# Performance work log

Measured on AMD Instinct MI355X. Metric: run time of the kernel, lower is better.

## Reference

```python
import jax, jax.numpy as jnp
import numpy as np

MIN_NORM = 1e-15
PROJ_EPS = 4e-3  # fp32 eps used by hgcn PoincareBall


def _artanh(x):
    x = jnp.clip(x, -1.0 + 1e-7, 1.0 - 1e-7)
    return 0.5 * jnp.log((1.0 + x) / (1.0 - x))


def _norm(x):
    return jnp.maximum(jnp.linalg.norm(x, axis=-1, keepdims=True), MIN_NORM)


def proj(x, c):
    norm = _norm(x)
    maxnorm = (1.0 - PROJ_EPS) / jnp.sqrt(c)
    return jnp.where(norm > maxnorm, x / norm * maxnorm, x)


def expmap0(u, c):
    sqrt_c = jnp.sqrt(c)
    u_norm = _norm(u)
    return jnp.tanh(sqrt_c * u_norm) * u / (sqrt_c * u_norm)


def logmap0(p, c):
    sqrt_c = jnp.sqrt(c)
    p_norm = _norm(p)
    return _artanh(sqrt_c * p_norm) * p / (sqrt_c * p_norm)


def mobius_add(x, y, c):
    x2 = jnp.sum(x * x, axis=-1, keepdims=True)
    y2 = jnp.sum(y * y, axis=-1, keepdims=True)
    xy = jnp.sum(x * y, axis=-1, keepdims=True)
    num = (1.0 + 2.0 * c * xy + c * y2) * x + (1.0 - c * x2) * y
    denom = 1.0 + 2.0 * c * xy + c * c * x2 * y2
    return num / jnp.maximum(denom, MIN_NORM)


def mobius_matvec(m, x, c):
    sqrt_c = jnp.sqrt(c)
    x_norm = _norm(x)
    mx = x @ m.T  # [N, out]
    mx_norm = _norm(mx)
    res_c = jnp.tanh(mx_norm / x_norm * _artanh(sqrt_c * x_norm)) * mx / (mx_norm * sqrt_c)
    cond = jnp.all(mx == 0.0, axis=-1, keepdims=True)
    return jnp.where(cond, jnp.zeros_like(res_c), res_c)


def setup_inputs() -> dict:
    key = jax.random.key(0)
    k1, k2, k3 = jax.random.split(key, 3)
    N, D = 8192, 256
    c = 1.0
    x = 0.05 * jax.random.normal(k1, (N, D), dtype=jnp.float32)
    x = proj(x, c)  # valid points on the Poincare ball
    # sparse-ish row-normalized adjacency, materialized densely
    a = (jax.random.uniform(k2, (N, N)) < 0.004).astype(jnp.float32)
    a = a + jnp.eye(N, dtype=jnp.float32)
    adj = a / jnp.sum(a, axis=-1, keepdims=True)
    gain = np.sqrt(2.0)
    bound = gain * np.sqrt(6.0 / (D + D))  # xavier_uniform with gain sqrt(2)
    weight = jax.random.uniform(k3, (D, D), minval=-bound, maxval=bound, dtype=jnp.float32)
    bias = jnp.zeros((D,), dtype=jnp.float32)
    return {"x": x, "adj": adj, "weight": weight, "bias": bias}


def reference(x, adj, weight, bias):
    c_in = jnp.float32(1.0)
    c_out = jnp.float32(1.0)
    # HypLinear (dropout=0, eval mode)
    mv = mobius_matvec(weight, x, c_in)
    res = proj(mv, c_in)
    hyp_bias = proj(expmap0(bias[None, :], c_in), c_in)  # proj_tan0 is identity
    h = proj(mobius_add(res, hyp_bias, c_in), c_in)
    # HypAgg (use_att=False): tangent-space neighborhood aggregation
    x_tangent = logmap0(h, c_in)
    support_t = adj @ x_tangent
    h = proj(expmap0(support_t, c_in), c_in)
    # HypAct
    xt = jax.nn.relu(logmap0(h, c_in))
    h = proj(expmap0(xt, c_out), c_out)
    return (h, adj)
```

## Files before the change

kernel.cpp:

```cpp
#include <hip/hip_runtime.h>
#include <hip/hip_bf16.h>

#define N_NODES 8192
#define D_DIM   256

typedef __attribute__((ext_vector_type(8))) short short8v;
typedef __attribute__((ext_vector_type(4))) float f32x4;

__device__ __forceinline__ float artanh_clip(float x) {
    x = fminf(x, 1.0f - 1e-7f);
    return 0.5f * logf((1.0f + x) / (1.0f - x));
}

__device__ __forceinline__ ushort4 cvt4_bf16(float4 v) {
    ushort4 b;
    b.x = __bfloat16_as_ushort(__float2bfloat16(v.x));
    b.y = __bfloat16_as_ushort(__float2bfloat16(v.y));
    b.z = __bfloat16_as_ushort(__float2bfloat16(v.z));
    b.w = __bfloat16_as_ushort(__float2bfloat16(v.w));
    return b;
}

__global__ void k0_bias(const float* __restrict__ bias, float* __restrict__ hbg) {
    __shared__ float sp[4];
    __shared__ float s_g;
    int t = threadIdx.x;
    float u = bias[t];
    float v = u * u;
    #pragma unroll
    for (int o = 1; o < 64; o <<= 1) v += __shfl_xor(v, o);
    if ((t & 63) == 0) sp[t >> 6] = v;
    __syncthreads();
    if (t == 0) {
        float s  = sp[0] + sp[1] + sp[2] + sp[3];
        float un = fmaxf(sqrtf(s), 1e-15f);
        float t1 = tanhf(un);
        s_g = (t1 > 0.996f) ? (0.996f / un) : (t1 / un);
    }
    __syncthreads();
    float hb = s_g * u;
    hbg[t] = hb;
    float v2 = hb * hb;
    #pragma unroll
    for (int o = 1; o < 64; o <<= 1) v2 += __shfl_xor(v2, o);
    if ((t & 63) == 0) sp[t >> 6] = v2;
    __syncthreads();
    if (t == 0) hbg[256] = sp[0] + sp[1] + sp[2] + sp[3];
}

__global__ __launch_bounds__(256) void k1_hyplinear(
    const float* __restrict__ x, const float* __restrict__ W,
    const float* __restrict__ hbg, __hip_bfloat16* __restrict__ xtT)
{
    __shared__ __align__(16) float sw[256][36];
    __shared__ __align__(16) float smx[16][260];
    __shared__ float s_xn[16], s_P[16], s_Q[16];
    __shared__ float s_hb[256];
    __shared__ float s_b2;

    const int t  = threadIdx.x;
    const int r0 = blockIdx.x * 16;

    s_hb[t] = hbg[t];
    if (t == 0) s_b2 = hbg[256];

    {
        int r = t >> 4, j = t & 15;
        const float* xp = x + (r0 + r) * 256 + j * 16;
        float s2 = 0.f;
        #pragma unroll
        for (int i = 0; i < 4; i++) {
            float4 v = *(const float4*)(xp + 4 * i);
            s2 += v.x * v.x + v.y * v.y + v.z * v.z + v.w * v.w;
        }
        s2 += __shfl_xor(s2, 1); s2 += __shfl_xor(s2, 2);
        s2 += __shfl_xor(s2, 4); s2 += __shfl_xor(s2, 8);
        if (j == 0) s_xn[r] = s2;
    }

    float acc[16];
    #pragma unroll
    for (int r = 0; r < 16; r++) acc[r] = 0.f;

    for (int kc = 0; kc < 8; kc++) {
        __syncthreads();
        {
            int c4 = (t & 7) * 4;
            #pragma unroll
            for (int i = 0; i < 8; i++) {
                int d = i * 32 + (t >> 3);
                *(float4*)(&sw[d][c4]) = *(const float4*)(W + d * 256 + kc * 32 + c4);
            }
        }
        __syncthreads();
        #pragma unroll
        for (int kk = 0; kk < 8; kk++) {
            float4 w4 = *(const float4*)(&sw[t][kk * 4]);
            #pragma unroll
            for (int r = 0; r < 16; r++) {
                const float4 xv = *(const float4*)(x + (r0 + r) * 256 + kc * 32 + kk * 4);
                acc[r] = fmaf(xv.x, w4.x, acc[r]);
                acc[r] = fmaf(xv.y, w4.y, acc[r]);
                acc[r] = fmaf(xv.z, w4.z, acc[r]);
                acc[r] = fmaf(xv.w, w4.w, acc[r]);
            }
        }
    }
    __syncthreads();
    #pragma unroll
    for (int r = 0; r < 16; r++) smx[r][t] = acc[r];
    __syncthreads();

    {
        int r = t >> 4, j = t & 15;
        float s2 = 0.f, dt = 0.f;
        #pragma unroll
        for (int i = 0; i < 16; i++) {
            float v = smx[r][j + 16 * i];
            s2 += v * v;
            dt += v * s_hb[j + 16 * i];
        }
        s2 += __shfl_xor(s2, 1); s2 += __shfl_xor(s2, 2);
        s2 += __shfl_xor(s2, 4); s2 += __shfl_xor(s2, 8);
        dt += __shfl_xor(dt, 1); dt += __shfl_xor(dt, 2);
        dt += __shfl_xor(dt, 4); dt += __shfl_xor(dt, 8);
        if (j == 0) {
            float b2  = s_b2;
            float xn  = fmaxf(sqrtf(s_xn[r]), 1e-15f);
            float mx2 = s2;
            float mxn = fmaxf(sqrtf(mx2), 1e-15f);
            float at = artanh_clip(xn);
            float tt = tanhf(mxn / xn * at);
            float fr = tt / mxn;
            if (tt > 0.996f) fr = 0.996f / mxn;
            float mvn = fminf(tt, 0.996f);
            float x2  = mvn * mvn;
            float xy  = fr * dt;
            float cA  = 1.0f + 2.0f * xy + b2;
            float cB  = 1.0f - x2;
            float den = fmaxf(1.0f + 2.0f * xy + x2 * b2, 1e-15f);
            float P0 = cA * fr / den;
            float Q0 = cB / den;
            float hn = sqrtf(fmaxf(P0 * P0 * mx2 + 2.0f * P0 * Q0 * dt + Q0 * Q0 * b2, 0.0f));
            hn = fmaxf(hn, 1e-15f);
            float pf  = (hn > 0.996f) ? (0.996f / hn) : 1.0f;
            float hnp = fminf(hn, 0.996f);
            float lam = artanh_clip(hnp) / hnp;
            s_P[r] = lam * pf * P0;
            s_Q[r] = lam * pf * Q0;
        }
    }
    __syncthreads();

    {
        float hb = s_hb[t];
        unsigned int pk[8];
        #pragma unroll
        for (int r = 0; r < 16; r += 2) {
            float a0 = s_P[r]     * acc[r]     + s_Q[r]     * hb;
            float a1 = s_P[r + 1] * acc[r + 1] + s_Q[r + 1] * hb;
            unsigned int lo = (unsigned int)__bfloat16_as_ushort(__float2bfloat16(a0));
            unsigned int hi = (unsigned int)__bfloat16_as_ushort(__float2bfloat16(a1));
            pk[r >> 1] = lo | (hi << 16);
        }
        uint4* dst = (uint4*)(xtT + t * 8192 + r0);
        dst[0] = make_uint4(pk[0], pk[1], pk[2], pk[3]);
        dst[1] = make_uint4(pk[4], pk[5], pk[6], pk[7]);
    }
}

__global__ __launch_bounds__(512) void k2_agg(
    const float* __restrict__ adj,
    const __hip_bfloat16* __restrict__ xtT,
    float* __restrict__ out_h,
    float* __restrict__ out_adj)
{
    __shared__ __align__(16) __hip_bfloat16 As[2][32][72];

    const int t     = threadIdx.x;
    const int lane  = t & 63;
    const int wave  = t >> 6;
    const int wr    = wave >> 2;
    const int wc    = wave & 3;
    const int bx    = blockIdx.x;
    const int m0    = (bx >> 2) * 32;
    const int kbase = (bx & 3) * 2048;

    const int srow = t >> 4;
    const int scol = (t & 15) * 4;
    const float* astage = adj     + (m0 + srow) * 8192 + kbase + scol;
    float*       ostage = out_adj + (m0 + srow) * 8192 + kbase + scol;

    const int arow = lane & 15;
    const int g8   = 8 * (lane >> 4);
    const int acol = wr * 32 + g8;
    const __hip_bfloat16* bptr = xtT + (wc * 64 + arow) * 8192 + kbase + wr * 32 + g8;

    f32x4 acc[8];
    #pragma unroll
    for (int i = 0; i < 8; i++) acc[i] = (f32x4){0.f, 0.f, 0.f, 0.f};

    {
        float4 v = *(const float4*)(astage);
        *(float4*)(ostage) = v;
        *(ushort4*)(&As[0][srow][scol]) = cvt4_bf16(v);
    }
    __syncthreads();

    for (int kt = 0; kt < 32; kt++) {
        const int cur = kt & 1;
        const bool hn = (kt + 1 < 32);
        float4 v;
        if (hn) v = *(const float4*)(astage + (kt + 1) * 64);

        const __hip_bfloat16* bb = bptr + kt * 64;
        short8v b0 = *(const short8v*)(bb);
        short8v b1 = *(const short8v*)(bb + 16 * 8192);
        short8v b2 = *(const short8v*)(bb + 32 * 8192);
        short8v b3 = *(const short8v*)(bb + 48 * 8192);
        short8v a0 = *(const short8v*)(&As[cur][arow][acol]);
        short8v a1 = *(const short8v*)(&As[cur][16 + arow][acol]);

        acc[0] = __builtin_amdgcn_mfma_f32_16x16x32_bf16(a0, b0, acc[0], 0, 0, 0);
        acc[1] = __builtin_amdgcn_mfma_f32_16x16x32_bf16(a0, b1, acc[1], 0, 0, 0);
        acc[2] = __builtin_amdgcn_mfma_f32_16x16x32_bf16(a0, b2, acc[2], 0, 0, 0);
        acc[3] = __builtin_amdgcn_mfma_f32_16x16x32_bf16(a0, b3, acc[3], 0, 0, 0);
        acc[4] = __builtin_amdgcn_mfma_f32_16x16x32_bf16(a1, b0, acc[4], 0, 0, 0);
        acc[5] = __builtin_amdgcn_mfma_f32_16x16x32_bf16(a1, b1, acc[5], 0, 0, 0);
        acc[6] = __builtin_amdgcn_mfma_f32_16x16x32_bf16(a1, b2, acc[6], 0, 0, 0);
        acc[7] = __builtin_amdgcn_mfma_f32_16x16x32_bf16(a1, b3, acc[7], 0, 0, 0);

        if (hn) {
            *(float4*)(ostage + (kt + 1) * 64) = v;
            *(ushort4*)(&As[cur ^ 1][srow][scol]) = cvt4_bf16(v);
        }
        __syncthreads();
    }

    const int crow0 = 4 * (lane >> 4);
    const int ccol  = lane & 15;
    #pragma unroll
    for (int mf = 0; mf < 2; mf++)
        #pragma unroll
        for (int nf = 0; nf < 4; nf++)
            #pragma unroll
            for (int q = 0; q < 4; q++)
                atomicAdd(out_h + (m0 + mf * 16 + crow0 + q) * 256 + wc * 64 + nf * 16 + ccol,
                          acc[mf * 4 + nf][q]);
}

__global__ __launch_bounds__(256) void k3_epilogue(float* __restrict__ h) {
    const int t = threadIdx.x;
    const int r = blockIdx.x * 16 + (t >> 4);
    const int j = t & 15;
    float* p = h + r * 256 + j * 16;

    float4 v[4];
    float s2 = 0.f, sp = 0.f;
    #pragma unroll
    for (int i = 0; i < 4; i++) {
        v[i] = *(const float4*)(p + 4 * i);
        s2 += v[i].x * v[i].x + v[i].y * v[i].y + v[i].z * v[i].z + v[i].w * v[i].w;
        float px = fmaxf(v[i].x, 0.f), py = fmaxf(v[i].y, 0.f);
        float pz = fmaxf(v[i].z, 0.f), pw = fmaxf(v[i].w, 0.f);
        sp += px * px + py * py + pz * pz + pw * pw;
    }
    s2 += __shfl_xor(s2, 1); s2 += __shfl_xor(s2, 2); s2 += __shfl_xor(s2, 4); s2 += __shfl_xor(s2, 8);
    sp += __shfl_xor(sp, 1); sp += __shfl_xor(sp, 2); sp += __shfl_xor(sp, 4); sp += __shfl_xor(sp, 8);

    float ns = fmaxf(sqrtf(s2), 1e-15f);
    float t1 = tanhf(ns);
    float alpha = (t1 > 0.996f) ? (0.996f / ns) : (t1 / ns);
    float nh = fminf(t1, 0.996f);
    float beta = artanh_clip(nh) / nh;
    float ba = beta * alpha;
    float nxt = fmaxf(ba * sqrtf(sp), 1e-15f);
    float t2 = tanhf(nxt);
    float delta = (t2 > 0.996f) ? (0.996f / nxt) : (t2 / nxt);
    float F = delta * ba;

    #pragma unroll
    for (int i = 0; i < 4; i++) {
        float4 o;
        o.x = F * fmaxf(v[i].x, 0.f);
        o.y = F * fmaxf(v[i].y, 0.f);
        o.z = F * fmaxf(v[i].z, 0.f);
        o.w = F * fmaxf(v[i].w, 0.f);
        *(float4*)(p + 4 * i) = o;
    }
}

extern "C" void kernel_launch(void* const* d_in, const int* in_sizes, int n_in,
                              void* d_out, int out_size, void* d_ws, size_t ws_size,
                              hipStream_t stream)
{
    const float* x    = (const float*)d_in[0];
    const float* adj  = (const float*)d_in[1];
    const float* W    = (const float*)d_in[2];
    const float* bias = (const float*)d_in[3];

    float* out_h   = (float*)d_out;
    float* out_adj = out_h + (size_t)N_NODES * D_DIM;

    __hip_bfloat16* xtT = (__hip_bfloat16*)d_ws;
    float* hbg = (float*)((char*)d_ws + (size_t)D_DIM * N_NODES * 2);

    k0_bias<<<1, 256, 0, stream>>>(bias, hbg);
    k1_hyplinear<<<512, 256, 0, stream>>>(x, W, hbg, xtT);
    hipMemsetAsync(out_h, 0, (size_t)N_NODES * D_DIM * sizeof(float), stream);
    k2_agg<<<1024, 512, 0, stream>>>(adj, xtT, out_h, out_adj);
    k3_epilogue<<<512, 256, 0, stream>>>(out_h);
}
```

Measured before the change: 304.8 us.

## Replace split-K atomic aggregation with column-tiled full-K GEMM and stage x in LDS

The aggregation kernel no longer splits K across four blocks with atomicAdd. Each block now covers a 32-row by 64-column output tile over the full K range and writes its result directly, so the memset is removed. The copy of adj to the output now uses nontemporal stores. In the linear kernel, x is staged once in shared memory instead of being re-read from global memory inside the FMA loop. The trade-off is that the four column blocks of each row tile each re-read the adj tile and each rewrite the same out_adj region, which multiplies the main memory traffic.

```diff
diff --git a/kernel.cpp b/kernel.cpp
--- a/kernel.cpp
+++ b/kernel.cpp
@@ -21,6 +21,11 @@
     return b;
 }
 
+__device__ __forceinline__ void nt_store4(float4 v, float* p) {
+    f32x4 w = {v.x, v.y, v.z, v.w};
+    __builtin_nontemporal_store(w, (f32x4*)p);
+}
+
 __global__ void k0_bias(const float* __restrict__ bias, float* __restrict__ hbg) {
     __shared__ float sp[4];
     __shared__ float s_g;
@@ -52,27 +57,32 @@
     const float* __restrict__ x, const float* __restrict__ W,
     const float* __restrict__ hbg, __hip_bfloat16* __restrict__ xtT)
 {
+    __shared__ __align__(16) float sx[16][264];
     __shared__ __align__(16) float sw[256][36];
-    __shared__ __align__(16) float smx[16][260];
     __shared__ float s_xn[16], s_P[16], s_Q[16];
     __shared__ float s_hb[256];
     __shared__ float s_b2;
 
     const int t  = threadIdx.x;
     const int r0 = blockIdx.x * 16;
-
+    const int row = t >> 4;
+    const int j16 = (t & 15) * 4;
+
+    {
+        #pragma unroll
+        for (int i = 0; i < 4; i++)
+            *(float4*)(&sx[row][j16 + 64 * i]) =
+                *(const float4*)(x + (r0 + row) * 256 + j16 + 64 * i);
+    }
     s_hb[t] = hbg[t];
     if (t == 0) s_b2 = hbg[256];
+    __syncthreads();
 
     {
         int r = t >> 4, j = t & 15;
-        const float* xp = x + (r0 + r) * 256 + j * 16;
         float s2 = 0.f;
         #pragma unroll
-        for (int i = 0; i < 4; i++) {
-            float4 v = *(const float4*)(xp + 4 * i);
-            s2 += v.x * v.x + v.y * v.y + v.z * v.z + v.w * v.w;
-        }
+        for (int i = 0; i < 16; i++) { float v = sx[r][j + 16 * i]; s2 += v * v; }
         s2 += __shfl_xor(s2, 1); s2 += __shfl_xor(s2, 2);
         s2 += __shfl_xor(s2, 4); s2 += __shfl_xor(s2, 8);
         if (j == 0) s_xn[r] = s2;
@@ -98,17 +108,17 @@
             float4 w4 = *(const float4*)(&sw[t][kk * 4]);
             #pragma unroll
             for (int r = 0; r < 16; r++) {
-                const float4 xv = *(const float4*)(x + (r0 + r) * 256 + kc * 32 + kk * 4);
-                acc[r] = fmaf(xv.x, w4.x, acc[r]);
-                acc[r] = fmaf(xv.y, w4.y, acc[r]);
-                acc[r] = fmaf(xv.z, w4.z, acc[r]);
-                acc[r] = fmaf(xv.w, w4.w, acc[r]);
+                float4 x4 = *(const float4*)(&sx[r][kc * 32 + kk * 4]);
+                acc[r] = fmaf(x4.x, w4.x, acc[r]);
+                acc[r] = fmaf(x4.y, w4.y, acc[r]);
+                acc[r] = fmaf(x4.z, w4.z, acc[r]);
+                acc[r] = fmaf(x4.w, w4.w, acc[r]);
             }
         }
     }
     __syncthreads();
     #pragma unroll
-    for (int r = 0; r < 16; r++) smx[r][t] = acc[r];
+    for (int r = 0; r < 16; r++) sx[r][t] = acc[r];
     __syncthreads();
 
     {
@@ -116,7 +126,7 @@
         float s2 = 0.f, dt = 0.f;
         #pragma unroll
         for (int i = 0; i < 16; i++) {
-            float v = smx[r][j + 16 * i];
+            float v = sx[r][j + 16 * i];
             s2 += v * v;
             dt += v * s_hb[j + 16 * i];
         }
@@ -177,61 +187,51 @@
 {
     __shared__ __align__(16) __hip_bfloat16 As[2][32][72];
 
-    const int t     = threadIdx.x;
-    const int lane  = t & 63;
-    const int wave  = t >> 6;
-    const int wr    = wave >> 2;
-    const int wc    = wave & 3;
-    const int bx    = blockIdx.x;
-    const int m0    = (bx >> 2) * 32;
-    const int kbase = (bx & 3) * 2048;
+    const int t    = threadIdx.x;
+    const int lane = t & 63;
+    const int wave = t >> 6;
+    const int wrh  = wave >> 2;
+    const int wc   = wave & 3;
+    const int bx   = blockIdx.x;
+    const int m    = (bx >> 5) * 8 + (bx & 7);
+    const int c    = (bx >> 3) & 3;
+    const int m0   = m * 32;
+    const int n0   = c * 64;
 
     const int srow = t >> 4;
     const int scol = (t & 15) * 4;
-    const float* astage = adj     + (m0 + srow) * 8192 + kbase + scol;
-    float*       ostage = out_adj + (m0 + srow) * 8192 + kbase + scol;
+    const float* astage = adj     + (m0 + srow) * 8192 + scol;
+    float*       ostage = out_adj + (m0 + srow) * 8192 + scol;
 
     const int arow = lane & 15;
     const int g8   = 8 * (lane >> 4);
-    const int acol = wr * 32 + g8;
-    const __hip_bfloat16* bptr = xtT + (wc * 64 + arow) * 8192 + kbase + wr * 32 + g8;
-
-    f32x4 acc[8];
-    #pragma unroll
-    for (int i = 0; i < 8; i++) acc[i] = (f32x4){0.f, 0.f, 0.f, 0.f};
+    const __hip_bfloat16* bptr = xtT + (n0 + wc * 16 + arow) * 8192 + g8;
+
+    f32x4 acc = (f32x4){0.f, 0.f, 0.f, 0.f};
 
     {
         float4 v = *(const float4*)(astage);
-        *(float4*)(ostage) = v;
+        nt_store4(v, ostage);
         *(ushort4*)(&As[0][srow][scol]) = cvt4_bf16(v);
     }
     __syncthreads();
 
-    for (int kt = 0; kt < 32; kt++) {
+    for (int kt = 0; kt < 128; kt++) {
         const int cur = kt & 1;
-        const bool hn = (kt + 1 < 32);
+        const bool hn = (kt + 1 < 128);
         float4 v;
         if (hn) v = *(const float4*)(astage + (kt + 1) * 64);
 
-        const __hip_bfloat16* bb = bptr + kt * 64;
-        short8v b0 = *(const short8v*)(bb);
-        short8v b1 = *(const short8v*)(bb + 16 * 8192);
-        short8v b2 = *(const short8v*)(bb + 32 * 8192);
-        short8v b3 = *(const short8v*)(bb + 48 * 8192);
-        short8v a0 = *(const short8v*)(&As[cur][arow][acol]);
-        short8v a1 = *(const short8v*)(&As[cur][16 + arow][acol]);
-
-        acc[0] = __builtin_amdgcn_mfma_f32_16x16x32_bf16(a0, b0, acc[0], 0, 0, 0);
-        acc[1] = __builtin_amdgcn_mfma_f32_16x16x32_bf16(a0, b1, acc[1], 0, 0, 0);
-        acc[2] = __builtin_amdgcn_mfma_f32_16x16x32_bf16(a0, b2, acc[2], 0, 0, 0);
-        acc[3] = __builtin_amdgcn_mfma_f32_16x16x32_bf16(a0, b3, acc[3], 0, 0, 0);
-        acc[4] = __builtin_amdgcn_mfma_f32_16x16x32_bf16(a1, b0, acc[4], 0, 0, 0);
-        acc[5] = __builtin_amdgcn_mfma_f32_16x16x32_bf16(a1, b1, acc[5], 0, 0, 0);
-        acc[6] = __builtin_amdgcn_mfma_f32_16x16x32_bf16(a1, b2, acc[6], 0, 0, 0);
-        acc[7] = __builtin_amdgcn_mfma_f32_16x16x32_bf16(a1, b3, acc[7], 0, 0, 0);
+        short8v b0 = *(const short8v*)(bptr + kt * 64);
+        short8v b1 = *(const short8v*)(bptr + kt * 64 + 32);
+        short8v a0 = *(const short8v*)(&As[cur][wrh * 16 + arow][g8]);
+        short8v a1 = *(const short8v*)(&As[cur][wrh * 16 + arow][32 + g8]);
+
+        acc = __builtin_amdgcn_mfma_f32_16x16x32_bf16(a0, b0, acc, 0, 0, 0);
+        acc = __builtin_amdgcn_mfma_f32_16x16x32_bf16(a1, b1, acc, 0, 0, 0);
 
         if (hn) {
-            *(float4*)(ostage + (kt + 1) * 64) = v;
+            nt_store4(v, ostage + (kt + 1) * 64);
             *(ushort4*)(&As[cur ^ 1][srow][scol]) = cvt4_bf16(v);
         }
         __syncthreads();
@@ -240,13 +240,8 @@
     const int crow0 = 4 * (lane >> 4);
     const int ccol  = lane & 15;
     #pragma unroll
-    for (int mf = 0; mf < 2; mf++)
-        #pragma unroll
-        for (int nf = 0; nf < 4; nf++)
-            #pragma unroll
-            for (int q = 0; q < 4; q++)
-                atomicAdd(out_h + (m0 + mf * 16 + crow0 + q) * 256 + wc * 64 + nf * 16 + ccol,
-                          acc[mf * 4 + nf][q]);
+    for (int q = 0; q < 4; q++)
+        out_h[(m0 + wrh * 16 + crow0 + q) * 256 + n0 + wc * 16 + ccol] = acc[q];
 }
 
 __global__ __launch_bounds__(256) void k3_epilogue(float* __restrict__ h) {
@@ -307,7 +302,6 @@
 
     k0_bias<<<1, 256, 0, stream>>>(bias, hbg);
     k1_hyplinear<<<512, 256, 0, stream>>>(x, W, hbg, xtT);
-    hipMemsetAsync(out_h, 0, (size_t)N_NODES * D_DIM * sizeof(float), stream);
     k2_agg<<<1024, 512, 0, stream>>>(adj, xtT, out_h, out_adj);
     k3_epilogue<<<512, 256, 0, stream>>>(out_h);
 }
```

After: 522.4 us. 1.71x slower.
